# Performance work log

Hardware: AMD Instinct MI355X
Metric: run time of the kernel (lower is better)

## Reference

```python
import jax, jax.numpy as jnp
import numpy as np

# Each of the 16 differentiable binary logic ops op_k(a,b) is a polynomial
# c0 + ca*a + cb*b + cab*(a*b). Rows follow the standard difflogic op table
# (op 3 = 'a' pass-through, matching the residual init in the source).
_OP2POLY = np.array([
    [0, 0, 0, 0],    # 0: False
    [0, 0, 0, 1],    # 1: a AND b
    [0, 1, 0, -1],   # 2: a AND NOT b
    [0, 1, 0, 0],    # 3: a
    [0, 0, 1, -1],   # 4: NOT a AND b
    [0, 0, 1, 0],    # 5: b
    [0, 1, 1, -2],   # 6: XOR
    [0, 1, 1, -1],   # 7: OR
    [1, -1, -1, 1],  # 8: NOR
    [1, -1, -1, 2],  # 9: XNOR
    [1, 0, -1, 0],   # 10: NOT b
    [1, 0, -1, 1],   # 11: a OR NOT b
    [1, -1, 0, 0],   # 12: NOT a
    [1, -1, 0, 1],   # 13: NOT a OR b
    [1, 0, 0, -1],   # 14: NAND
    [1, 0, 0, 0],    # 15: True
], dtype=np.float32)

KERNEL_SIZE, STRIDE, PADDING, GROUPS, TREE_DEPTH, TAU = 3, 1, 1, 1, 4, 1.0


def setup_inputs() -> dict:
    key = jax.random.key(0)
    k0, k1, k2, k3, k4 = jax.random.split(key, 5)
    B, Cin, H, W = 16, 64, 64, 64
    OC, N = 128, 2 ** TREE_DEPTH
    x = jax.random.uniform(k0, (B, Cin, H, W), dtype=jnp.float32)
    weights = jax.random.normal(k1, (OC, N - 1, 16), dtype=jnp.float32)
    ci = jax.random.randint(k2, (OC, N), 0, Cin // GROUPS, dtype=jnp.int32)
    px = jax.random.randint(k3, (OC, N), 0, KERNEL_SIZE, dtype=jnp.int32)
    py = jax.random.randint(k4, (OC, N), 0, KERNEL_SIZE, dtype=jnp.int32)
    return {"x": x, "weights": weights, "input_channel_indices": ci,
            "input_pos_x_indices": px, "input_pos_y_indices": py}


def _forward(x, weights, ci, px, py):
    B, Cin, H, W = x.shape
    OC = weights.shape[0]
    N = 2 ** TREE_DEPTH
    # Training-mode weights with straight-through estimator:
    # value = one_hot(argmax), gradient flows through softmax.
    w_soft = jax.nn.softmax(weights / TAU, axis=-1).astype(x.dtype)
    w_hard = jax.nn.one_hot(jnp.argmax(weights, axis=-1), 16, dtype=x.dtype)
    w = w_soft + jax.lax.stop_gradient(w_hard - w_soft)
    # [OC, num_gates, 4] polynomial coefficients over (1, a, b, ab)
    coeffs = jnp.einsum('ogk,kc->ogc', w, jnp.asarray(_OP2POLY, x.dtype))

    xp = jnp.pad(x, ((0, 0), (0, 0), (PADDING, PADDING), (PADDING, PADDING)))
    oh = (H + 2 * PADDING - KERNEL_SIZE) // STRIDE + 1
    ow = (W + 2 * PADDING - KERNEL_SIZE) // STRIDE + 1

    icpg = Cin // GROUPS
    group_of_oc = jnp.arange(OC, dtype=jnp.int32) // (OC // GROUPS)
    chan = group_of_oc[:, None] * icpg + ci                       # [OC, N]
    rows = (jnp.arange(oh, dtype=jnp.int32) * STRIDE)[None, None, :] + py[:, :, None]  # [OC,N,oh]
    cols = (jnp.arange(ow, dtype=jnp.int32) * STRIDE)[None, None, :] + px[:, :, None]  # [OC,N,ow]
    # Irregular per-output gather: [B, OC, N, oh, ow]
    vals = xp[:, chan[:, :, None, None], rows[:, :, :, None], cols[:, :, None, :]]

    # Binary tree of logic gates, level by level (gates stored leaf-level first).
    gate_off = 0
    for _ in range(TREE_DEPTH):
        n = vals.shape[2] // 2
        a, b = vals[:, :, 0::2], vals[:, :, 1::2]
        cc = coeffs[:, gate_off:gate_off + n]                     # [OC, n, 4]
        c0, ca, cb, cab = (cc[None, :, :, i, None, None] for i in range(4))
        vals = c0 + ca * a + cb * b + cab * (a * b)
        gate_off += n
    y = vals[:, :, 0]                                             # [B, OC, oh, ow]

    # 2x2 OR-pool (soft OR = 1 - prod(1 - v)), floor division of spatial dims.
    ph, pw = oh // 2, ow // 2
    y = y[:, :, :ph * 2, :pw * 2].reshape(B, OC, ph, 2, pw, 2)
    return 1.0 - jnp.prod(1.0 - y, axis=(3, 5))


def reference(x, weights, input_channel_indices, input_pos_x_indices, input_pos_y_indices):
    return _forward(x, weights, input_channel_indices, input_pos_x_indices, input_pos_y_indices)
```

## Files before the change

kernel.cpp:

```cpp
#include <hip/hip_runtime.h>

#define BATCH 16
#define CIN   64
#define H_    64
#define W_    64
#define IMG   (H_ * W_)
#define OCH   128
#define NLEAF 16
#define NGATE 15
#define PH    32
#define PW    32

#define C_STRIDE_F4 16
#define DESC_OFF    8192
#define WS_NEED_BYTES ((DESC_OFF + OCH * NLEAF) * 4)

#define ZF     24576
#define SMEM_F (ZF + 384)

typedef float f2 __attribute__((ext_vector_type(2)));

__device__ __constant__ __align__(16) float OP2POLY[16][4] = {
    {0, 0, 0, 0}, {0, 0, 0, 1}, {0, 1, 0, -1}, {0, 1, 0, 0},
    {0, 0, 1, -1}, {0, 0, 1, 0}, {0, 1, 1, -2}, {0, 1, 1, -1},
    {1, -1, -1, 1}, {1, -1, -1, 2}, {1, 0, -1, 0}, {1, 0, -1, 1},
    {1, -1, 0, 0}, {1, -1, 0, 1}, {1, 0, 0, -1}, {1, 0, 0, 0}};

__global__ __launch_bounds__(1024) void prep(
    const float* __restrict__ weights,
    const int* __restrict__ ci,
    const int* __restrict__ px,
    const int* __restrict__ py,
    float* __restrict__ ws)
{
    int t = blockIdx.x * 1024 + threadIdx.x;
    if (t < OCH * NGATE) {
        const float* wp = weights + t * 16;
        int best = 0;
        float bv = wp[0];
#pragma unroll
        for (int k = 1; k < 16; ++k) {
            float v = wp[k];
            if (v > bv) { bv = v; best = k; }
        }
        int oc = t / 15, g = t - oc * 15;
        reinterpret_cast<float4*>(ws)[oc * C_STRIDE_F4 + g] =
            reinterpret_cast<const float4*>(OP2POLY)[best];
    } else if (t < OCH * NGATE + OCH * NLEAF) {
        int t2 = t - OCH * NGATE;
        int ch = ci[t2], pyy = py[t2], pxx = px[t2];
        ((int*)ws)[DESC_OFF + t2] = ((ch * 384 + pyy * 64) << 4) | (pyy << 2) | pxx;
    }
}

__global__ __launch_bounds__(1024) void logic_tree_main(
    const float* __restrict__ x,
    const float* __restrict__ ws,
    float* __restrict__ out)
{
    __shared__ float smem[SMEM_F];

    const int blk = blockIdx.x;
    const int xcd = blk & 7;
    const int j   = blk >> 3;
    const int b   = (xcd << 1) | (j >> 4);
    const int strip = j & 15;
    const int r0  = strip << 2;
    const int tid = threadIdx.x;

    const float4* xb4 = reinterpret_cast<const float4*>(x + (size_t)b * (CIN * IMG));
#pragma unroll
    for (int i = 0; i < 6; ++i) {
        int fidx = tid + i * 1024;
        int ch   = fidx / 96;
        int rem  = fidx - ch * 96;
        int row  = rem >> 4;
        int c4   = rem & 15;
        int gr   = r0 - 1 + row;
        float4 val = make_float4(0.f, 0.f, 0.f, 0.f);
        if ((unsigned)gr < (unsigned)H_)
            val = xb4[((ch << 6) | gr) * 16 + c4];
        *reinterpret_cast<float4*>(&smem[fidx * 4]) = val;
    }
    if (tid < 384) smem[ZF + tid] = 0.0f;
    __syncthreads();

    const int wave = tid >> 6;
    const int lane = tid & 63;

#pragma unroll 1
    for (int q = 0; q < 8; ++q) {
        const int oc = __builtin_amdgcn_readfirstlane(wave * 8 + q);
        const float4* C4 = reinterpret_cast<const float4*>(ws) + oc * C_STRIDE_F4;
        const int*    D  = ((const int*)ws) + DESC_OFF + oc * NLEAF;

        int base[NLEAF];
#pragma unroll
        for (int n = 0; n < NLEAF; ++n) {
            int d  = D[n];
            int c  = lane + (d & 3) - 1;
            int ccl = min(max(c, 0), W_ - 1);
            int bin = (d >> 4) + ccl;
            int bz  = ZF + ((d >> 2) & 3) * 64 + lane;
            base[n] = (c == ccl) ? bin : bz;
        }

        const size_t obase =
            (((size_t)b * OCH + oc) * PH + (strip << 1)) * PW + (lane >> 1);

#pragma unroll
        for (int rp = 0; rp < 2; ++rp) {
            f2 v[NLEAF];
#pragma unroll
            for (int n = 0; n < NLEAF; ++n) {
                v[n].x = smem[base[n] + rp * 128];
                v[n].y = smem[base[n] + rp * 128 + 64];
            }
            int go = 0;
#pragma unroll
            for (int lev = 8; lev >= 1; lev >>= 1) {
#pragma unroll
                for (int t = 0; t < lev; ++t) {
                    const float4 cc = C4[go + t];
                    f2 a  = v[2 * t];
                    f2 bb = v[2 * t + 1];
                    v[t] = cc.x + cc.y * a + cc.z * bb + cc.w * (a * bb);
                }
                go += lev;
            }
            float p  = (1.0f - v[0].x) * (1.0f - v[0].y);
            float pp = p * __shfl_xor(p, 1, 64);
            if (!(lane & 1))
                out[obase + (size_t)rp * PW] = 1.0f - pp;
        }
    }
}

extern "C" void kernel_launch(void* const* d_in, const int* in_sizes, int n_in,
                              void* d_out, int out_size, void* d_ws, size_t ws_size,
                              hipStream_t stream) {
    const float* x       = (const float*)d_in[0];
    const float* weights = (const float*)d_in[1];
    const int*   ci      = (const int*)d_in[2];
    const int*   px      = (const int*)d_in[3];
    const int*   py      = (const int*)d_in[4];
    float* out = (float*)d_out;
    float* ws  = (float*)d_ws;

    prep<<<4, 1024, 0, stream>>>(weights, ci, px, py, ws);
    logic_tree_main<<<BATCH * 16, 1024, 0, stream>>>(x, ws, out);
}
```

Baseline: 98.80 us.

## Pad shared-memory rows with zero halo and process four output rows per thread

Stages the input strip into shared memory with 66-float padded rows and a zero halo, so each leaf address becomes a single precomputed offset instead of per-leaf clamping and zero-buffer selection. Each thread now evaluates the gate tree on four rows at once using a 4-wide vector, where before it made two passes of two rows. The final store writes from all lanes, with each lane selecting which pooled row it outputs. The wider vectors increase register pressure, and the odd row stride changes the shared-memory bank pattern.

After: 90.76 us. -8.1%, faster.

```diff
diff --git a/kernel.cpp b/kernel.cpp
--- a/kernel.cpp
+++ b/kernel.cpp
@@ -13,12 +13,14 @@
 
 #define C_STRIDE_F4 16
 #define DESC_OFF    8192
-#define WS_NEED_BYTES ((DESC_OFF + OCH * NLEAF) * 4)
 
-#define ZF     24576
-#define SMEM_F (ZF + 384)
+#define ROWS   6
+#define RSTR   66
+#define CHSTR  (ROWS * RSTR)
+#define XSB    2
+#define SMEM_F (XSB + CIN * CHSTR)
 
-typedef float f2 __attribute__((ext_vector_type(2)));
+typedef float f4v __attribute__((ext_vector_type(4)));
 
 __device__ __constant__ __align__(16) float OP2POLY[16][4] = {
     {0, 0, 0, 0}, {0, 0, 0, 1}, {0, 1, 0, -1}, {0, 1, 0, 0},
@@ -48,12 +50,12 @@
             reinterpret_cast<const float4*>(OP2POLY)[best];
     } else if (t < OCH * NGATE + OCH * NLEAF) {
         int t2 = t - OCH * NGATE;
-        int ch = ci[t2], pyy = py[t2], pxx = px[t2];
-        ((int*)ws)[DESC_OFF + t2] = ((ch * 384 + pyy * 64) << 4) | (pyy << 2) | pxx;
+        ((int*)ws)[DESC_OFF + t2] =
+            XSB + ci[t2] * CHSTR + py[t2] * RSTR + px[t2] - 1;
     }
 }
 
-__global__ __launch_bounds__(1024) void logic_tree_main(
+__global__ __launch_bounds__(1024, 4) void logic_tree_main(
     const float* __restrict__ x,
     const float* __restrict__ ws,
     float* __restrict__ out)
@@ -68,21 +70,26 @@
     const int r0  = strip << 2;
     const int tid = threadIdx.x;
 
-    const float4* xb4 = reinterpret_cast<const float4*>(x + (size_t)b * (CIN * IMG));
+    const float2* xb2 =
+        reinterpret_cast<const float2*>(x + (size_t)b * (CIN * IMG));
 #pragma unroll
-    for (int i = 0; i < 6; ++i) {
-        int fidx = tid + i * 1024;
-        int ch   = fidx / 96;
-        int rem  = fidx - ch * 96;
-        int row  = rem >> 4;
-        int c4   = rem & 15;
-        int gr   = r0 - 1 + row;
-        float4 val = make_float4(0.f, 0.f, 0.f, 0.f);
+    for (int i = 0; i < 12; ++i) {
+        int f   = tid + i * 1024;
+        int ch  = f / 192;
+        int rem = f - ch * 192;
+        int row = rem >> 5;
+        int c2  = rem & 31;
+        int gr  = r0 - 1 + row;
+        float2 val = make_float2(0.f, 0.f);
         if ((unsigned)gr < (unsigned)H_)
-            val = xb4[((ch << 6) | gr) * 16 + c4];
-        *reinterpret_cast<float4*>(&smem[fidx * 4]) = val;
+            val = xb2[((ch << 6) | gr) * 32 + c2];
+        *reinterpret_cast<float2*>(&smem[XSB + ch * CHSTR + row * RSTR + c2 * 2]) = val;
     }
-    if (tid < 384) smem[ZF + tid] = 0.0f;
+    if (tid < 770) {
+        int idx = (tid < 768) ? (XSB + (tid >> 1) * RSTR + 64 + (tid & 1))
+                              : (tid - 768);
+        smem[idx] = 0.0f;
+    }
     __syncthreads();
 
     const int wave = tid >> 6;
@@ -94,45 +101,36 @@
         const float4* C4 = reinterpret_cast<const float4*>(ws) + oc * C_STRIDE_F4;
         const int*    D  = ((const int*)ws) + DESC_OFF + oc * NLEAF;
 
-        int base[NLEAF];
+        f4v v[NLEAF];
 #pragma unroll
         for (int n = 0; n < NLEAF; ++n) {
-            int d  = D[n];
-            int c  = lane + (d & 3) - 1;
-            int ccl = min(max(c, 0), W_ - 1);
-            int bin = (d >> 4) + ccl;
-            int bz  = ZF + ((d >> 2) & 3) * 64 + lane;
-            base[n] = (c == ccl) ? bin : bz;
+            const int base = D[n] + lane;
+            v[n].x = smem[base];
+            v[n].y = smem[base + RSTR];
+            v[n].z = smem[base + 2 * RSTR];
+            v[n].w = smem[base + 3 * RSTR];
         }
 
-        const size_t obase =
-            (((size_t)b * OCH + oc) * PH + (strip << 1)) * PW + (lane >> 1);
+        int go = 0;
+#pragma unroll
+        for (int lev = 8; lev >= 1; lev >>= 1) {
+#pragma unroll
+            for (int t = 0; t < lev; ++t) {
+                const float4 cc = C4[go + t];
+                f4v a  = v[2 * t];
+                f4v bb = v[2 * t + 1];
+                v[t] = cc.x + cc.y * a + cc.z * bb + cc.w * (a * bb);
+            }
+            go += lev;
+        }
 
-#pragma unroll
-        for (int rp = 0; rp < 2; ++rp) {
-            f2 v[NLEAF];
-#pragma unroll
-            for (int n = 0; n < NLEAF; ++n) {
-                v[n].x = smem[base[n] + rp * 128];
-                v[n].y = smem[base[n] + rp * 128 + 64];
-            }
-            int go = 0;
-#pragma unroll
-            for (int lev = 8; lev >= 1; lev >>= 1) {
-#pragma unroll
-                for (int t = 0; t < lev; ++t) {
-                    const float4 cc = C4[go + t];
-                    f2 a  = v[2 * t];
-                    f2 bb = v[2 * t + 1];
-                    v[t] = cc.x + cc.y * a + cc.z * bb + cc.w * (a * bb);
-                }
-                go += lev;
-            }
-            float p  = (1.0f - v[0].x) * (1.0f - v[0].y);
-            float pp = p * __shfl_xor(p, 1, 64);
-            if (!(lane & 1))
-                out[obase + (size_t)rp * PW] = 1.0f - pp;
-        }
+        float p0 = (1.0f - v[0].x) * (1.0f - v[0].y);
+        float p1 = (1.0f - v[0].z) * (1.0f - v[0].w);
+        float q0 = p0 * __shfl_xor(p0, 1, 64);
+        float q1 = p1 * __shfl_xor(p1, 1, 64);
+        float val = (lane & 1) ? (1.0f - q1) : (1.0f - q0);
+        out[(((size_t)b * OCH + oc) * PH + (strip << 1) + (lane & 1)) * PW +
+            (lane >> 1)] = val;
     }
 }
 
```
